# Optimization experiments

Hardware: AMD Instinct MI355X
Metric: run time of the kernel (lower is better)

The kernel has to match this reference:

```python
import jax, jax.numpy as jnp
import numpy as np

NEG = -1e30  # safe log-zero for fp32/bf16


def _ctc_neg_log_likelihood(labels, log_probs, label_length, data_length, blank):
    """Standard CTC alpha (forward) DP in log space.
    labels: [B, L] int, log_probs: [T, B, C], lengths: [B] int.
    Returns per-example negative log likelihood [B]."""
    T, B, C = log_probs.shape
    L = labels.shape[1]
    S = 2 * L + 1  # extended label: blank, l1, blank, l2, ..., blank
    ext = jnp.full((B, S), blank, dtype=labels.dtype).at[:, 1::2].set(labels)
    prev2 = jnp.concatenate([jnp.full((B, 2), -1, labels.dtype), ext[:, :-2]], axis=1)
    allow_skip = (ext != blank) & (ext != prev2)  # [B, S] skip-transition legality

    def emit(lp_t):  # [B, C] -> [B, S]
        return jnp.take_along_axis(lp_t, ext, axis=1)

    # t = 0: paths can only be at s=0 (blank) or s=1 (first label)
    alpha0 = jnp.where(jnp.arange(S)[None, :] < 2, emit(log_probs[0]), NEG)

    def step(alpha, xs):
        lp_t, t = xs
        a1 = jnp.concatenate([jnp.full((B, 1), NEG, alpha.dtype), alpha[:, :-1]], axis=1)
        a2 = jnp.concatenate([jnp.full((B, 2), NEG, alpha.dtype), alpha[:, :-2]], axis=1)
        a2 = jnp.where(allow_skip, a2, NEG)
        new = jax.nn.logsumexp(jnp.stack([alpha, a1, a2]), axis=0) + emit(lp_t)
        # freeze alpha once past this example's sequence length
        return jnp.where((t < data_length)[:, None], new, alpha), None

    alpha, _ = jax.lax.scan(step, alpha0, (log_probs[1:], jnp.arange(1, T)))

    # likelihood = alpha[2*len] (final blank) + alpha[2*len - 1] (final label)
    a_blank = jnp.take_along_axis(alpha, (2 * label_length)[:, None], axis=1)[:, 0]
    a_label = jnp.take_along_axis(alpha, (2 * label_length - 1)[:, None], axis=1)[:, 0]
    return -jnp.logaddexp(a_blank, a_label)


def setup_inputs() -> dict:
    key = jax.random.key(0)
    k1, k2, k3, k4 = jax.random.split(key, 4)
    T, B, C, L = 1024, 32, 1024, 128
    data = jax.random.normal(k1, (T, B, C), dtype=jnp.float32)
    labels = jax.random.randint(k2, (B, L), 1, C, dtype=jnp.int32)  # avoid blank=0
    label_length = jax.random.randint(k3, (B,), 64, L + 1, dtype=jnp.int32)
    data_length = jax.random.randint(k4, (B,), 512, T + 1, dtype=jnp.int32)
    return {"labels": labels, "data": data, "label_length": label_length,
            "data_length": data_length}


def reference(labels, data, label_length, data_length):
    # from_logits=True -> ctc_loss_v2: log_softmax then CTC; blank_index=0
    log_probs = jax.nn.log_softmax(data, axis=-1)
    loss = _ctc_neg_log_likelihood(labels, log_probs, label_length, data_length, 0)
    return jnp.mean(loss).reshape([1])
```

## Files before the change

### kernel.cpp

```cpp
#include <hip/hip_runtime.h>
#include <hip/hip_bf16.h>

#define T_DIM 1024
#define B_DIM 32
#define C_DIM 1024
#define L_DIM 128
#define S_DIM 257

__global__ __launch_bounds__(256) void emit_kernel(const float* __restrict__ data,
                                                   const int* __restrict__ labels,
                                                   float2* __restrict__ epair,
                                                   float* __restrict__ eblank) {
    const int wave = threadIdx.x >> 6;
    const int lane = threadIdx.x & 63;
    const int row = blockIdx.x * 4 + wave;
    const int b = row & (B_DIM - 1);
    const int t = row >> 5;

    const float4* d4 = (const float4*)(data + (size_t)row * C_DIM);
    float4 v[4];
    float m = -3.4e38f;
#pragma unroll
    for (int k = 0; k < 4; ++k) {
        v[k] = d4[lane + 64 * k];
        m = fmaxf(m, fmaxf(fmaxf(v[k].x, v[k].y), fmaxf(v[k].z, v[k].w)));
    }
#pragma unroll
    for (int off = 32; off >= 1; off >>= 1)
        m = fmaxf(m, __shfl_xor(m, off, 64));
    float s = 0.f;
#pragma unroll
    for (int k = 0; k < 4; ++k)
        s += __expf(v[k].x - m) + __expf(v[k].y - m) +
             __expf(v[k].z - m) + __expf(v[k].w - m);
#pragma unroll
    for (int off = 32; off >= 1; off >>= 1)
        s += __shfl_xor(s, off, 64);
    const float lse = m + __logf(s);

    const float* drow = data + (size_t)row * C_DIM;
    const int2 cc = ((const int2*)(labels + b * L_DIM))[lane];
    float2 pr;
    pr.x = __expf(drow[cc.x] - lse);
    pr.y = __expf(drow[cc.y] - lse);
    epair[(size_t)row * 64 + lane] = pr;
    if (lane == 0) eblank[b * T_DIM + t] = __expf(drow[0] - lse);
}

__global__ __launch_bounds__(64) void dp_kernel(const float2* __restrict__ epair,
                                                const float* __restrict__ eblank,
                                                const int* __restrict__ labels,
                                                const int* __restrict__ label_length,
                                                const int* __restrict__ data_length,
                                                float* __restrict__ out) {
    const int b = blockIdx.x;
    const int l = threadIdx.x;
    const int* lab = labels + b * L_DIM;
    const int len = label_length[b];
    const int dlen = data_length[b];

    const int2 cc = ((const int2*)lab)[l];
    const int cprev = (l > 0) ? lab[2 * l - 1] : -1;
    const bool skip1 = (l > 0) && (cc.x != cprev);
    const bool skip3 = (cc.y != cc.x);

    const float* ebrow = eblank + b * T_DIM;

    double a0, a1, a2 = 0.0, a3 = 0.0, a4 = 0.0;
    {
        const float2 e0 = epair[(size_t)b * 64 + l];
        const float eb0 = ebrow[0];
        a0 = (l == 0) ? (double)eb0 : 0.0;
        a1 = (l == 0) ? (double)e0.x : 0.0;
    }
    long long kacc = 0;

    auto step = [&](float2 epv, float ebv) {
        const double e1 = (double)epv.x, e2 = (double)epv.y, eb = (double)ebv;
        double h = __shfl_up(a3, 1, 64);
        if (l == 0) h = 0.0;
        const double n0 = (a0 + h) * eb;
        const double n1 = (a1 + a0 + (skip1 ? h : 0.0)) * e1;
        const double n2 = (a2 + a1) * eb;
        const double n3 = (a3 + a2 + (skip3 ? a1 : 0.0)) * e2;
        const double n4 = (a4 + a3) * eb;
        a0 = n0; a1 = n1; a2 = n2; a3 = n3; a4 = n4;
    };

    auto renorm = [&]() {
        double m = fmax(fmax(fmax(a0, a1), fmax(a2, a3)), a4);
#pragma unroll
        for (int off = 32; off >= 1; off >>= 1)
            m = fmax(m, __shfl_xor(m, off, 64));
        const long long mb = __double_as_longlong(m);
        const int ex = (int)((mb >> 52) & 0x7ff) - 1023;
        const double sc = __longlong_as_double((long long)(1023 - ex) << 52);
        a0 *= sc; a1 *= sc; a2 *= sc; a3 *= sc; a4 *= sc;
        kacc += ex;
    };

    float2 bufA[8], bufB[8];
    float ebA[8], ebB[8];

    auto load_chunk = [&](int c, float2* ep8, float* eb8) {
#pragma unroll
        for (int j = 0; j < 8; ++j) {
            int t = 1 + 8 * c + j;
            int tc = (t < T_DIM) ? t : (T_DIM - 1);
            ep8[j] = epair[(size_t)(tc * B_DIM + b) * 64 + l];
            eb8[j] = ebrow[tc];
        }
    };

    auto compute_chunk = [&](int c, const float2* ep8, const float* eb8) {
        const int t0 = 1 + 8 * c;
        if (t0 + 7 < dlen) {
#pragma unroll
            for (int j = 0; j < 8; ++j) step(ep8[j], eb8[j]);
        } else {
#pragma unroll
            for (int j = 0; j < 8; ++j)
                if (t0 + j < dlen) step(ep8[j], eb8[j]);
        }
    };

    const int nch = (dlen - 1 + 7) / 8;
    load_chunk(0, bufA, ebA);
    for (int c = 0; c < nch; c += 2) {
        load_chunk(c + 1, bufB, ebB);
        compute_chunk(c, bufA, ebA);
        load_chunk(c + 2, bufA, ebA);
        compute_chunk(c + 1, bufB, ebB);
        if (((c + 1) & 3) == 3) renorm();
    }

    __shared__ double fin[S_DIM];
    fin[4 * l + 0] = a0; fin[4 * l + 1] = a1;
    fin[4 * l + 2] = a2; fin[4 * l + 3] = a3;
    if (l == 63) fin[256] = a4;
    __syncthreads();
    if (l == 0) {
        const double v = fin[2 * len] + fin[2 * len - 1];
        const long long vb = __double_as_longlong(v);
        const int ve = (int)((vb >> 52) & 0x7ff) - 1023;
        const double mant = __longlong_as_double(
            (vb & 0x000FFFFFFFFFFFFFLL) | (1023LL << 52));
        const double l2 = (double)__log2f((float)mant) + (double)ve + (double)kacc;
        const float loss = (float)(-l2 * 0.6931471805599453);
        atomicAdd(out, loss * (1.0f / B_DIM));
    }
}

extern "C" void kernel_launch(void* const* d_in, const int* in_sizes, int n_in,
                              void* d_out, int out_size, void* d_ws, size_t ws_size,
                              hipStream_t stream) {
    const int*   labels       = (const int*)d_in[0];
    const float* data         = (const float*)d_in[1];
    const int*   label_length = (const int*)d_in[2];
    const int*   data_length  = (const int*)d_in[3];
    float*       out          = (float*)d_out;

    float2* epair  = (float2*)d_ws;
    float*  eblank = (float*)((char*)d_ws + (size_t)T_DIM * B_DIM * 64 * sizeof(float2));

    hipMemsetAsync(d_out, 0, sizeof(float), stream);

    const int rows = T_DIM * B_DIM;
    emit_kernel<<<rows / 4, 256, 0, stream>>>(data, labels, epair, eblank);
    dp_kernel<<<B_DIM, 64, 0, stream>>>(epair, eblank, labels, label_length,
                                        data_length, out);
}
```

Measured before the change: 287.7 us.

## Deepen DP prefetch to 16-step chunks with sched barriers and padded buffers

The serial DP kernel now loads 16 timesteps per chunk instead of 8 and issues each buffer's loads a full chunk ahead. Scheduling barriers stop the compiler from sinking those loads, which is meant to hide global-load latency on the serial critical path. Workspace rows are padded so the clamp on over-read indices can be dropped. The select-based skip terms become FMAs, renormalisation now runs every two chunks, and the atomic mean is replaced by a small final reduction kernel, which adds one launch and removes the memset. Padded tail entries are read without being written, but those steps are masked out by the data-length check.

```diff
diff --git a/kernel.cpp b/kernel.cpp
--- a/kernel.cpp
+++ b/kernel.cpp
@@ -6,6 +6,7 @@
 #define C_DIM 1024
 #define L_DIM 128
 #define S_DIM 257
+#define TPAD  (T_DIM + 64)
 
 __global__ __launch_bounds__(256) void emit_kernel(const float* __restrict__ data,
                                                    const int* __restrict__ labels,
@@ -44,15 +45,15 @@
     pr.x = __expf(drow[cc.x] - lse);
     pr.y = __expf(drow[cc.y] - lse);
     epair[(size_t)row * 64 + lane] = pr;
-    if (lane == 0) eblank[b * T_DIM + t] = __expf(drow[0] - lse);
+    if (lane == 0) eblank[b * TPAD + t] = __expf(drow[0] - lse);
 }
 
-__global__ __launch_bounds__(64) void dp_kernel(const float2* __restrict__ epair,
-                                                const float* __restrict__ eblank,
-                                                const int* __restrict__ labels,
-                                                const int* __restrict__ label_length,
-                                                const int* __restrict__ data_length,
-                                                float* __restrict__ out) {
+__global__ __launch_bounds__(64, 1) void dp_kernel(const float2* __restrict__ epair,
+                                                   const float* __restrict__ eblank,
+                                                   const int* __restrict__ labels,
+                                                   const int* __restrict__ label_length,
+                                                   const int* __restrict__ data_length,
+                                                   float* __restrict__ lossbuf) {
     const int b = blockIdx.x;
     const int l = threadIdx.x;
     const int* lab = labels + b * L_DIM;
@@ -61,10 +62,10 @@
 
     const int2 cc = ((const int2*)lab)[l];
     const int cprev = (l > 0) ? lab[2 * l - 1] : -1;
-    const bool skip1 = (l > 0) && (cc.x != cprev);
-    const bool skip3 = (cc.y != cc.x);
+    const double skip1d = ((l > 0) && (cc.x != cprev)) ? 1.0 : 0.0;
+    const double skip3d = (cc.y != cc.x) ? 1.0 : 0.0;
 
-    const float* ebrow = eblank + b * T_DIM;
+    const float* ebrow = eblank + b * TPAD;
 
     double a0, a1, a2 = 0.0, a3 = 0.0, a4 = 0.0;
     {
@@ -80,9 +81,9 @@
         double h = __shfl_up(a3, 1, 64);
         if (l == 0) h = 0.0;
         const double n0 = (a0 + h) * eb;
-        const double n1 = (a1 + a0 + (skip1 ? h : 0.0)) * e1;
+        const double n1 = fma(skip1d, h, a1 + a0) * e1;
         const double n2 = (a2 + a1) * eb;
-        const double n3 = (a3 + a2 + (skip3 ? a1 : 0.0)) * e2;
+        const double n3 = fma(skip3d, a1, a3 + a2) * e2;
         const double n4 = (a4 + a3) * eb;
         a0 = n0; a1 = n1; a2 = n2; a3 = n3; a4 = n4;
     };
@@ -99,39 +100,42 @@
         kacc += ex;
     };
 
-    float2 bufA[8], bufB[8];
-    float ebA[8], ebB[8];
+    float2 bufA[16], bufB[16];
+    float ebA[16], ebB[16];
 
-    auto load_chunk = [&](int c, float2* ep8, float* eb8) {
+    auto load_chunk = [&](int c, float2* ep, float* eb) {
+        const int t0 = 1 + 16 * c;
 #pragma unroll
-        for (int j = 0; j < 8; ++j) {
-            int t = 1 + 8 * c + j;
-            int tc = (t < T_DIM) ? t : (T_DIM - 1);
-            ep8[j] = epair[(size_t)(tc * B_DIM + b) * 64 + l];
-            eb8[j] = ebrow[tc];
+        for (int j = 0; j < 16; ++j) {
+            ep[j] = epair[(size_t)((t0 + j) * B_DIM + b) * 64 + l];
+            eb[j] = ebrow[t0 + j];
         }
     };
 
-    auto compute_chunk = [&](int c, const float2* ep8, const float* eb8) {
-        const int t0 = 1 + 8 * c;
-        if (t0 + 7 < dlen) {
+    auto compute_chunk = [&](int c, const float2* ep, const float* eb) {
+        const int t0 = 1 + 16 * c;
+        if (t0 + 15 < dlen) {
 #pragma unroll
-            for (int j = 0; j < 8; ++j) step(ep8[j], eb8[j]);
+            for (int j = 0; j < 16; ++j) step(ep[j], eb[j]);
         } else {
 #pragma unroll
-            for (int j = 0; j < 8; ++j)
-                if (t0 + j < dlen) step(ep8[j], eb8[j]);
+            for (int j = 0; j < 16; ++j)
+                if (t0 + j < dlen) step(ep[j], eb[j]);
         }
     };
 
-    const int nch = (dlen - 1 + 7) / 8;
+    const int nch = (dlen - 1 + 15) / 16;
     load_chunk(0, bufA, ebA);
+    load_chunk(1, bufB, ebB);
+    __builtin_amdgcn_sched_barrier(0);
     for (int c = 0; c < nch; c += 2) {
-        load_chunk(c + 1, bufB, ebB);
         compute_chunk(c, bufA, ebA);
         load_chunk(c + 2, bufA, ebA);
+        __builtin_amdgcn_sched_barrier(0);
         compute_chunk(c + 1, bufB, ebB);
-        if (((c + 1) & 3) == 3) renorm();
+        load_chunk(c + 3, bufB, ebB);
+        __builtin_amdgcn_sched_barrier(0);
+        renorm();
     }
 
     __shared__ double fin[S_DIM];
@@ -146,9 +150,18 @@
         const double mant = __longlong_as_double(
             (vb & 0x000FFFFFFFFFFFFFLL) | (1023LL << 52));
         const double l2 = (double)__log2f((float)mant) + (double)ve + (double)kacc;
-        const float loss = (float)(-l2 * 0.6931471805599453);
-        atomicAdd(out, loss * (1.0f / B_DIM));
+        lossbuf[b] = (float)(-l2 * 0.6931471805599453);
     }
+}
+
+__global__ __launch_bounds__(64) void final_kernel(const float* __restrict__ lossbuf,
+                                                   float* __restrict__ out) {
+    const int l = threadIdx.x;
+    float v = (l < B_DIM) ? lossbuf[l] : 0.f;
+#pragma unroll
+    for (int off = 32; off >= 1; off >>= 1)
+        v += __shfl_xor(v, off, 64);
+    if (l == 0) out[0] = v * (1.0f / B_DIM);
 }
 
 extern "C" void kernel_launch(void* const* d_in, const int* in_sizes, int n_in,
@@ -161,12 +174,12 @@
     float*       out          = (float*)d_out;
 
     float2* epair  = (float2*)d_ws;
-    float*  eblank = (float*)((char*)d_ws + (size_t)T_DIM * B_DIM * 64 * sizeof(float2));
-
-    hipMemsetAsync(d_out, 0, sizeof(float), stream);
+    float*  eblank = (float*)((char*)d_ws + (size_t)TPAD * B_DIM * 64 * sizeof(float2));
+    float*  lossb  = eblank + (size_t)B_DIM * TPAD;
 
     const int rows = T_DIM * B_DIM;
     emit_kernel<<<rows / 4, 256, 0, stream>>>(data, labels, epair, eblank);
     dp_kernel<<<B_DIM, 64, 0, stream>>>(epair, eblank, labels, label_length,
-                                        data_length, out);
+                                        data_length, lossb);
+    final_kernel<<<1, 64, 0, stream>>>(lossb, out);
 }
```

Measured after the change: 271.3 us. 1.06x faster.
